# Kernel tuning notes

Hardware: AMD Instinct MI355X
Metric: run time of the kernel (lower is better)

## Reference

```python
import jax, jax.numpy as jnp
import numpy as np

B, N, D = 16, 2048, 128

def setup_inputs() -> dict:
    key = jax.random.key(0)
    kq, kk, kv = jax.random.split(key, 3)
    q = jax.random.normal(kq, (B, N, D), dtype=jnp.float32)
    k = jax.random.normal(kk, (B, N, D), dtype=jnp.float32)
    v = jax.random.normal(kv, (B, N, D), dtype=jnp.float32)
    return {"q": q, "k": k, "v": v}

def reference(q, k, v):
    # attn = softmax(q @ k^T, axis=2)   (NOTE: no temperature scaling, matching source)
    scores = jnp.einsum("bnd,bmd->bnm", q, k)  # [B, N, N]
    attn = jax.nn.softmax(scores, axis=2)
    # dropout p=0.0 -> identity
    output = jnp.einsum("bnm,bmd->bnd", attn, v)  # [B, N, D]
    return (output, attn)
```

## Files before the change

kernel.cpp:

```cpp
#include <hip/hip_runtime.h>

#define N 2048
#define D 128
#define BB 16

typedef __attribute__((ext_vector_type(8))) short s16x8;
typedef __attribute__((ext_vector_type(4))) float f32x4;

__device__ __forceinline__ void split2(float x0, float x1, unsigned& h, unsigned& l) {
    unsigned b0 = __float_as_uint(x0), b1 = __float_as_uint(x1);
    float r0 = x0 - __uint_as_float(b0 & 0xffff0000u);
    float r1 = x1 - __uint_as_float(b1 & 0xffff0000u);
    h = (b0 >> 16) | (b1 & 0xffff0000u);
    l = (__float_as_uint(r0) >> 16) | (__float_as_uint(r1) & 0xffff0000u);
}

__global__ __launch_bounds__(256) void zero_kernel(float4* __restrict__ p, int n4) {
    int i = blockIdx.x * 256 + threadIdx.x;
    const int stride = gridDim.x * 256;
    for (; i < n4; i += stride) p[i] = make_float4(0.f, 0.f, 0.f, 0.f);
}

__global__ __launch_bounds__(256) void qk_kernel(const float* __restrict__ q,
                                                 const float* __restrict__ k,
                                                 float* __restrict__ attn,
                                                 float* __restrict__ outp) {
    __shared__ unsigned short Qh[128 * 32], Ql[128 * 32];
    __shared__ unsigned short Kh[128 * 32], Kl[128 * 32];
    const int t  = threadIdx.x;
    const int b  = blockIdx.z;
    const int ib = blockIdx.y * 128;
    const int jb = blockIdx.x * 128;
    const float* qp = q + ((size_t)b * N + ib) * D;
    const float* kp = k + ((size_t)b * N + jb) * D;

    const int lane = t & 63;
    const int w    = t >> 6;
    const int wr   = (w >> 1) * 64;
    const int wc   = (w & 1) * 64;
    const int l15  = lane & 15;
    const int l4   = lane >> 4;

    f32x4 acc[4][4] = {};

    for (int ks = 0; ks < 4; ++ks) {
        __syncthreads();
        #pragma unroll
        for (int c = 0; c < 4; ++c) {
            int flat = c * 256 + t;
            int row  = flat >> 3;
            int f4   = flat & 7;
            float4 qv = *(const float4*)(qp + (size_t)row * D + ks * 32 + f4 * 4);
            float4 kv = *(const float4*)(kp + (size_t)row * D + ks * 32 + f4 * 4);
            int idx = row * 32 + (((f4 >> 1) ^ (row & 3)) * 8) + (f4 & 1) * 4;
            uint2 hh, ll;
            split2(qv.x, qv.y, hh.x, ll.x);
            split2(qv.z, qv.w, hh.y, ll.y);
            *(uint2*)(Qh + idx) = hh;
            *(uint2*)(Ql + idx) = ll;
            split2(kv.x, kv.y, hh.x, ll.x);
            split2(kv.z, kv.w, hh.y, ll.y);
            *(uint2*)(Kh + idx) = hh;
            *(uint2*)(Kl + idx) = ll;
        }
        __syncthreads();

        s16x8 ah[4], al[4], bh[4], bl[4];
        #pragma unroll
        for (int ti = 0; ti < 4; ++ti) {
            int row = wr + ti * 16 + l15;
            int idx = row * 32 + ((l4 ^ (row & 3)) * 8);
            ah[ti] = *(const s16x8*)(Qh + idx);
            al[ti] = *(const s16x8*)(Ql + idx);
        }
        #pragma unroll
        for (int tj = 0; tj < 4; ++tj) {
            int row = wc + tj * 16 + l15;
            int idx = row * 32 + ((l4 ^ (row & 3)) * 8);
            bh[tj] = *(const s16x8*)(Kh + idx);
            bl[tj] = *(const s16x8*)(Kl + idx);
        }
        #pragma unroll
        for (int ti = 0; ti < 4; ++ti)
            #pragma unroll
            for (int tj = 0; tj < 4; ++tj) {
                acc[ti][tj] = __builtin_amdgcn_mfma_f32_16x16x32_bf16(ah[ti], bh[tj], acc[ti][tj], 0, 0, 0);
                acc[ti][tj] = __builtin_amdgcn_mfma_f32_16x16x32_bf16(ah[ti], bl[tj], acc[ti][tj], 0, 0, 0);
                acc[ti][tj] = __builtin_amdgcn_mfma_f32_16x16x32_bf16(al[ti], bh[tj], acc[ti][tj], 0, 0, 0);
            }
    }

    #pragma unroll
    for (int ti = 0; ti < 4; ++ti) {
        #pragma unroll
        for (int r = 0; r < 4; ++r) {
            int row = ib + wr + ti * 16 + l4 * 4 + r;
            float* arow = attn + ((size_t)b * N + row) * N + jb + wc;
            float rs = 0.f;
            #pragma unroll
            for (int tj = 0; tj < 4; ++tj) {
                float e = __expf(acc[ti][tj][r]);
                arow[tj * 16 + l15] = e;
                rs += e;
            }
            rs += __shfl_xor(rs, 1);
            rs += __shfl_xor(rs, 2);
            rs += __shfl_xor(rs, 4);
            rs += __shfl_xor(rs, 8);
            if (l15 == 0) atomicAdd(outp + ((size_t)b * N + row) * D, rs);
        }
    }
}

__global__ __launch_bounds__(256) void pv_kernel(const float* __restrict__ v,
                                                 float* __restrict__ attn,
                                                 float* __restrict__ outp) {
    __shared__ unsigned short Ph[64 * 64], Pl[64 * 64];
    __shared__ unsigned short Vth[128 * 64], Vtl[128 * 64];
    __shared__ float invs[64];
    const int t  = threadIdx.x;
    const int b  = blockIdx.y;
    const int ib = blockIdx.x * 64;
    float* ap       = attn + ((size_t)b * N + ib) * N;
    const float* vp = v + (size_t)b * N * D;
    float* op       = outp + ((size_t)b * N + ib) * D;

    if (t < 64) invs[t] = 1.0f / op[(size_t)t * D];

    const int lane = t & 63;
    const int w    = t >> 6;
    const int rg   = (w >> 1) * 32;
    const int dg   = (w & 1) * 64;
    const int l15  = lane & 15;
    const int l4   = lane >> 4;

    f32x4 acc[2][4] = {};

    float4 pe[4], va[4], vb[4];
    #pragma unroll
    for (int c = 0; c < 4; ++c) {
        int flat = c * 256 + t;
        pe[c] = *(const float4*)(ap + (size_t)(flat >> 4) * N + (flat & 15) * 4);
        int jp = flat >> 5, d4 = flat & 31;
        va[c] = *(const float4*)(vp + (size_t)(jp * 2) * D + d4 * 4);
        vb[c] = *(const float4*)(vp + (size_t)(jp * 2 + 1) * D + d4 * 4);
    }

    for (int jc = 0; jc < 32; ++jc) {
        __syncthreads();
        #pragma unroll
        for (int c = 0; c < 4; ++c) {
            int flat = c * 256 + t;
            int row = flat >> 4, j4 = flat & 15;
            float iv = invs[row];
            float4 p4;
            p4.x = pe[c].x * iv; p4.y = pe[c].y * iv;
            p4.z = pe[c].z * iv; p4.w = pe[c].w * iv;
            *(float4*)(ap + (size_t)row * N + jc * 64 + j4 * 4) = p4;
            uint2 hh, ll;
            split2(p4.x, p4.y, hh.x, ll.x);
            split2(p4.z, p4.w, hh.y, ll.y);
            int idx = row * 64 + (((j4 >> 1) ^ (row & 7)) * 8) + (j4 & 1) * 4;
            *(uint2*)(Ph + idx) = hh;
            *(uint2*)(Pl + idx) = ll;
        }
        #pragma unroll
        for (int c = 0; c < 4; ++c) {
            int flat = c * 256 + t;
            int jp = flat >> 5, d4 = flat & 31;
            int j = jp * 2;
            float4 v0 = va[c], v1 = vb[c];
            #pragma unroll
            for (int e = 0; e < 4; ++e) {
                float x0 = (&v0.x)[e], x1 = (&v1.x)[e];
                unsigned h, l;
                split2(x0, x1, h, l);
                int d = d4 * 4 + e;
                int idx = d * 64 + (((j >> 3) ^ (d & 7)) * 8) + (j & 7);
                *(unsigned*)(Vth + idx) = h;
                *(unsigned*)(Vtl + idx) = l;
            }
        }
        __syncthreads();
        if (jc < 31) {
            #pragma unroll
            for (int c = 0; c < 4; ++c) {
                int flat = c * 256 + t;
                pe[c] = *(const float4*)(ap + (size_t)(flat >> 4) * N + (jc + 1) * 64 + (flat & 15) * 4);
                int jp = flat >> 5, d4 = flat & 31;
                va[c] = *(const float4*)(vp + (size_t)((jc + 1) * 64 + jp * 2) * D + d4 * 4);
                vb[c] = *(const float4*)(vp + (size_t)((jc + 1) * 64 + jp * 2 + 1) * D + d4 * 4);
            }
        }
        #pragma unroll
        for (int ksj = 0; ksj < 2; ++ksj) {
            s16x8 pah[2], pal[2], bh[4], bl[4];
            #pragma unroll
            for (int ti = 0; ti < 2; ++ti) {
                int row = rg + ti * 16 + l15;
                int idx = row * 64 + (((ksj * 4 + l4) ^ (row & 7)) * 8);
                pah[ti] = *(const s16x8*)(Ph + idx);
                pal[ti] = *(const s16x8*)(Pl + idx);
            }
            #pragma unroll
            for (int tj = 0; tj < 4; ++tj) {
                int d = dg + tj * 16 + l15;
                int idx = d * 64 + (((ksj * 4 + l4) ^ (d & 7)) * 8);
                bh[tj] = *(const s16x8*)(Vth + idx);
                bl[tj] = *(const s16x8*)(Vtl + idx);
            }
            #pragma unroll
            for (int ti = 0; ti < 2; ++ti)
                #pragma unroll
                for (int tj = 0; tj < 4; ++tj) {
                    acc[ti][tj] = __builtin_amdgcn_mfma_f32_16x16x32_bf16(pah[ti], bh[tj], acc[ti][tj], 0, 0, 0);
                    acc[ti][tj] = __builtin_amdgcn_mfma_f32_16x16x32_bf16(pah[ti], bl[tj], acc[ti][tj], 0, 0, 0);
                    acc[ti][tj] = __builtin_amdgcn_mfma_f32_16x16x32_bf16(pal[ti], bh[tj], acc[ti][tj], 0, 0, 0);
                }
        }
    }

    #pragma unroll
    for (int ti = 0; ti < 2; ++ti)
        #pragma unroll
        for (int r = 0; r < 4; ++r) {
            int row = rg + ti * 16 + l4 * 4 + r;
            #pragma unroll
            for (int tj = 0; tj < 4; ++tj)
                op[(size_t)row * D + dg + tj * 16 + l15] = acc[ti][tj][r];
        }
}

extern "C" void kernel_launch(void* const* d_in, const int* in_sizes, int n_in,
                              void* d_out, int out_size, void* d_ws, size_t ws_size,
                              hipStream_t stream) {
    const float* q = (const float*)d_in[0];
    const float* k = (const float*)d_in[1];
    const float* v = (const float*)d_in[2];
    float* out  = (float*)d_out;
    float* attn = out + (size_t)BB * N * D;

    zero_kernel<<<1024, 256, 0, stream>>>((float4*)out, BB * N * D / 4);
    qk_kernel<<<dim3(N / 128, N / 128, BB), 256, 0, stream>>>(q, k, attn, out);
    pv_kernel<<<dim3(N / 64, BB), 256, 0, stream>>>(v, attn, out);
}
```

Measured before the change: 596.0 us.

## Precompute transposed bf16 hi/lo split of V in workspace for PV kernel

Adds a small pre-pass kernel that splits V into bf16 high and low parts and stores them transposed (D-major) in workspace. The PV kernel then loads the pre-split, transposed V tiles with vector loads and writes them straight into swizzled shared memory. This removes the per-block split and scattered transposing LDS writes that were repeated by every row-block of each batch. The cost is an extra kernel launch, workspace traffic, and a fallback path when the workspace is too small.

Measured after the change: 712.0 us. 1.19x slower.

```diff
diff --git a/kernel.cpp b/kernel.cpp
--- a/kernel.cpp
+++ b/kernel.cpp
@@ -19,6 +19,29 @@
     int i = blockIdx.x * 256 + threadIdx.x;
     const int stride = gridDim.x * 256;
     for (; i < n4; i += stride) p[i] = make_float4(0.f, 0.f, 0.f, 0.f);
+}
+
+__global__ __launch_bounds__(256) void vt_kernel(const float* __restrict__ v,
+                                                 unsigned short* __restrict__ vth,
+                                                 unsigned short* __restrict__ vtl) {
+    const int t    = threadIdx.x;
+    const int lane = t & 63;
+    const int w    = t >> 6;
+    const int b    = blockIdx.z;
+    const int n0   = blockIdx.x * 32 + w * 8;
+    const int d    = blockIdx.y * 64 + lane;
+    const float* vp = v + ((size_t)b * N + n0) * D + d;
+    float x[8];
+    #pragma unroll
+    for (int i = 0; i < 8; ++i) x[i] = vp[(size_t)i * D];
+    uint4 h, l;
+    split2(x[0], x[1], h.x, l.x);
+    split2(x[2], x[3], h.y, l.y);
+    split2(x[4], x[5], h.z, l.z);
+    split2(x[6], x[7], h.w, l.w);
+    size_t idx = ((size_t)b * D + d) * N + n0;
+    *(uint4*)(vth + idx) = h;
+    *(uint4*)(vtl + idx) = l;
 }
 
 __global__ __launch_bounds__(256) void qk_kernel(const float* __restrict__ q,
@@ -112,18 +135,20 @@
     }
 }
 
-__global__ __launch_bounds__(256) void pv_kernel(const float* __restrict__ v,
-                                                 float* __restrict__ attn,
-                                                 float* __restrict__ outp) {
+__global__ __launch_bounds__(256) void pv_pre_kernel(const unsigned short* __restrict__ vth,
+                                                     const unsigned short* __restrict__ vtl,
+                                                     float* __restrict__ attn,
+                                                     float* __restrict__ outp) {
     __shared__ unsigned short Ph[64 * 64], Pl[64 * 64];
-    __shared__ unsigned short Vth[128 * 64], Vtl[128 * 64];
+    __shared__ unsigned short Vh[128 * 64], Vl[128 * 64];
     __shared__ float invs[64];
     const int t  = threadIdx.x;
     const int b  = blockIdx.y;
     const int ib = blockIdx.x * 64;
-    float* ap       = attn + ((size_t)b * N + ib) * N;
-    const float* vp = v + (size_t)b * N * D;
-    float* op       = outp + ((size_t)b * N + ib) * D;
+    float* ap = attn + ((size_t)b * N + ib) * N;
+    const unsigned short* vhp = vth + (size_t)b * D * N;
+    const unsigned short* vlp = vtl + (size_t)b * D * N;
+    float* op = outp + ((size_t)b * N + ib) * D;
 
     if (t < 64) invs[t] = 1.0f / op[(size_t)t * D];
 
@@ -136,14 +161,14 @@
 
     f32x4 acc[2][4] = {};
 
-    float4 pe[4], va[4], vb[4];
+    float4 pe[4], fh[4], fl[4];
     #pragma unroll
     for (int c = 0; c < 4; ++c) {
         int flat = c * 256 + t;
         pe[c] = *(const float4*)(ap + (size_t)(flat >> 4) * N + (flat & 15) * 4);
-        int jp = flat >> 5, d4 = flat & 31;
-        va[c] = *(const float4*)(vp + (size_t)(jp * 2) * D + d4 * 4);
-        vb[c] = *(const float4*)(vp + (size_t)(jp * 2 + 1) * D + d4 * 4);
+        int d = flat >> 3, g = flat & 7;
+        fh[c] = *(const float4*)(vhp + (size_t)d * N + g * 8);
+        fl[c] = *(const float4*)(vlp + (size_t)d * N + g * 8);
     }
 
     for (int jc = 0; jc < 32; ++jc) {
@@ -167,6 +192,116 @@
         #pragma unroll
         for (int c = 0; c < 4; ++c) {
             int flat = c * 256 + t;
+            int d = flat >> 3, g = flat & 7;
+            int sidx = d * 64 + ((g ^ (d & 7)) * 8);
+            *(float4*)(Vh + sidx) = fh[c];
+            *(float4*)(Vl + sidx) = fl[c];
+        }
+        __syncthreads();
+        if (jc < 31) {
+            #pragma unroll
+            for (int c = 0; c < 4; ++c) {
+                int flat = c * 256 + t;
+                pe[c] = *(const float4*)(ap + (size_t)(flat >> 4) * N + (jc + 1) * 64 + (flat & 15) * 4);
+                int d = flat >> 3, g = flat & 7;
+                fh[c] = *(const float4*)(vhp + (size_t)d * N + (jc + 1) * 64 + g * 8);
+                fl[c] = *(const float4*)(vlp + (size_t)d * N + (jc + 1) * 64 + g * 8);
+            }
+        }
+        #pragma unroll
+        for (int ksj = 0; ksj < 2; ++ksj) {
+            s16x8 pah[2], pal[2], bh[4], bl[4];
+            #pragma unroll
+            for (int ti = 0; ti < 2; ++ti) {
+                int row = rg + ti * 16 + l15;
+                int idx = row * 64 + (((ksj * 4 + l4) ^ (row & 7)) * 8);
+                pah[ti] = *(const s16x8*)(Ph + idx);
+                pal[ti] = *(const s16x8*)(Pl + idx);
+            }
+            #pragma unroll
+            for (int tj = 0; tj < 4; ++tj) {
+                int d = dg + tj * 16 + l15;
+                int idx = d * 64 + (((ksj * 4 + l4) ^ (d & 7)) * 8);
+                bh[tj] = *(const s16x8*)(Vh + idx);
+                bl[tj] = *(const s16x8*)(Vl + idx);
+            }
+            #pragma unroll
+            for (int ti = 0; ti < 2; ++ti)
+                #pragma unroll
+                for (int tj = 0; tj < 4; ++tj) {
+                    acc[ti][tj] = __builtin_amdgcn_mfma_f32_16x16x32_bf16(pah[ti], bh[tj], acc[ti][tj], 0, 0, 0);
+                    acc[ti][tj] = __builtin_amdgcn_mfma_f32_16x16x32_bf16(pah[ti], bl[tj], acc[ti][tj], 0, 0, 0);
+                    acc[ti][tj] = __builtin_amdgcn_mfma_f32_16x16x32_bf16(pal[ti], bh[tj], acc[ti][tj], 0, 0, 0);
+                }
+        }
+    }
+
+    #pragma unroll
+    for (int ti = 0; ti < 2; ++ti)
+        #pragma unroll
+        for (int r = 0; r < 4; ++r) {
+            int row = rg + ti * 16 + l4 * 4 + r;
+            #pragma unroll
+            for (int tj = 0; tj < 4; ++tj)
+                op[(size_t)row * D + dg + tj * 16 + l15] = acc[ti][tj][r];
+        }
+}
+
+__global__ __launch_bounds__(256) void pv_fb_kernel(const float* __restrict__ v,
+                                                    float* __restrict__ attn,
+                                                    float* __restrict__ outp) {
+    __shared__ unsigned short Ph[64 * 64], Pl[64 * 64];
+    __shared__ unsigned short Vth[128 * 64], Vtl[128 * 64];
+    __shared__ float invs[64];
+    const int t  = threadIdx.x;
+    const int b  = blockIdx.y;
+    const int ib = blockIdx.x * 64;
+    float* ap       = attn + ((size_t)b * N + ib) * N;
+    const float* vp = v + (size_t)b * N * D;
+    float* op       = outp + ((size_t)b * N + ib) * D;
+
+    if (t < 64) invs[t] = 1.0f / op[(size_t)t * D];
+
+    const int lane = t & 63;
+    const int w    = t >> 6;
+    const int rg   = (w >> 1) * 32;
+    const int dg   = (w & 1) * 64;
+    const int l15  = lane & 15;
+    const int l4   = lane >> 4;
+
+    f32x4 acc[2][4] = {};
+
+    float4 pe[4], va[4], vb[4];
+    #pragma unroll
+    for (int c = 0; c < 4; ++c) {
+        int flat = c * 256 + t;
+        pe[c] = *(const float4*)(ap + (size_t)(flat >> 4) * N + (flat & 15) * 4);
+        int jp = flat >> 5, d4 = flat & 31;
+        va[c] = *(const float4*)(vp + (size_t)(jp * 2) * D + d4 * 4);
+        vb[c] = *(const float4*)(vp + (size_t)(jp * 2 + 1) * D + d4 * 4);
+    }
+
+    for (int jc = 0; jc < 32; ++jc) {
+        __syncthreads();
+        #pragma unroll
+        for (int c = 0; c < 4; ++c) {
+            int flat = c * 256 + t;
+            int row = flat >> 4, j4 = flat & 15;
+            float iv = invs[row];
+            float4 p4;
+            p4.x = pe[c].x * iv; p4.y = pe[c].y * iv;
+            p4.z = pe[c].z * iv; p4.w = pe[c].w * iv;
+            *(float4*)(ap + (size_t)row * N + jc * 64 + j4 * 4) = p4;
+            uint2 hh, ll;
+            split2(p4.x, p4.y, hh.x, ll.x);
+            split2(p4.z, p4.w, hh.y, ll.y);
+            int idx = row * 64 + (((j4 >> 1) ^ (row & 7)) * 8) + (j4 & 1) * 4;
+            *(uint2*)(Ph + idx) = hh;
+            *(uint2*)(Pl + idx) = ll;
+        }
+        #pragma unroll
+        for (int c = 0; c < 4; ++c) {
+            int flat = c * 256 + t;
             int jp = flat >> 5, d4 = flat & 31;
             int j = jp * 2;
             float4 v0 = va[c], v1 = vb[c];
@@ -240,7 +375,18 @@
     float* out  = (float*)d_out;
     float* attn = out + (size_t)BB * N * D;
 
+    const size_t vt_elems = (size_t)BB * D * N;
+    const bool use_ws = ws_size >= vt_elems * 2 * sizeof(unsigned short);
+
     zero_kernel<<<1024, 256, 0, stream>>>((float4*)out, BB * N * D / 4);
-    qk_kernel<<<dim3(N / 128, N / 128, BB), 256, 0, stream>>>(q, k, attn, out);
-    pv_kernel<<<dim3(N / 64, BB), 256, 0, stream>>>(v, attn, out);
-}
+    if (use_ws) {
+        unsigned short* vth = (unsigned short*)d_ws;
+        unsigned short* vtl = vth + vt_elems;
+        vt_kernel<<<dim3(N / 32, 2, BB), 256, 0, stream>>>(v, vth, vtl);
+        qk_kernel<<<dim3(N / 128, N / 128, BB), 256, 0, stream>>>(q, k, attn, out);
+        pv_pre_kernel<<<dim3(N / 64, BB), 256, 0, stream>>>(vth, vtl, attn, out);
+    } else {
+        qk_kernel<<<dim3(N / 128, N / 128, BB), 256, 0, stream>>>(q, k, attn, out);
+        pv_fb_kernel<<<dim3(N / 64, BB), 256, 0, stream>>>(v, attn, out);
+    }
+}
```
